# Kernel optimization log

Measured on AMD Instinct MI355X. Metric: run time of the kernel, lower is better.

## Reference

```python
import jax, jax.numpy as jnp
import numpy as np

N = 100_000      # nodes
E = 800_000      # edges (avg degree 8)
IN = 64          # in_channels
OUT = 64         # out_channels
HEADS = 4
HD = OUT // HEADS  # per-head out channels (concat=True)


def _unif(key, shape, fan_in):
    b = 1.0 / np.sqrt(fan_in)
    return jax.random.uniform(key, shape, jnp.float32, -b, b)


def setup_inputs() -> dict:
    key = jax.random.key(0)
    ks = jax.random.split(key, 12)
    x = jax.random.normal(ks[0], (N, IN), jnp.float32)
    pos = jax.random.normal(ks[1], (N, 3), jnp.float32)
    edge_index = jax.random.randint(ks[2], (2, E), 0, N, jnp.int32)
    # Per-head PointTransformerConv params (stacked over heads).
    # lin / lin_src / lin_dst are bias-free Linear(in, hd); pos_nn is Linear(3, hd) with bias.
    W_lin = _unif(ks[3], (HEADS, IN, HD), IN)
    W_src = _unif(ks[4], (HEADS, IN, HD), IN)
    W_dst = _unif(ks[5], (HEADS, IN, HD), IN)
    W_pos = _unif(ks[6], (HEADS, 3, HD), 3)
    b_pos = _unif(ks[7], (HEADS, HD), 3)
    # projection MLP: Linear(OUT,OUT) -> ReLU -> Linear(OUT,OUT)
    W1 = _unif(ks[8], (OUT, OUT), OUT)
    b1 = _unif(ks[9], (OUT,), OUT)
    W2 = _unif(ks[10], (OUT, OUT), OUT)
    b2 = _unif(ks[11], (OUT,), OUT)
    return dict(x=x, pos=pos, edge_index=edge_index, W_lin=W_lin, W_src=W_src,
                W_dst=W_dst, W_pos=W_pos, b_pos=b_pos, W1=W1, b1=b1, W2=W2, b2=b2)


def reference(x, pos, edge_index, W_lin, W_src, W_dst, W_pos, b_pos, W1, b1, W2, b2):
    # Add self-loops (PointTransformerConv default add_self_loops=True).
    loops = jnp.arange(N, dtype=edge_index.dtype)
    src = jnp.concatenate([edge_index[0], loops])   # j (source)
    dst = jnp.concatenate([edge_index[1], loops])   # i (target)

    # Per-node, all-heads projections: [N, H, HD]
    v = jnp.einsum('ni,hio->nho', x, W_lin)
    a_src = jnp.einsum('ni,hio->nho', x, W_src)
    a_dst = jnp.einsum('ni,hio->nho', x, W_dst)

    # Relative-position encoding delta = pos_nn(pos_i - pos_j): [Et, H, HD]
    rel = pos[dst] - pos[src]
    delta = jnp.einsum('ec,hco->eho', rel, W_pos) + b_pos

    # Attention logits per edge/channel: alpha_i - alpha_j + delta
    alpha = a_dst[dst] - a_src[src] + delta

    # Segment softmax over incoming edges of each target node (numerically stable).
    amax = jax.ops.segment_max(alpha, dst, num_segments=N)
    amax = jnp.where(jnp.isfinite(amax), amax, 0.0)
    ex = jnp.exp(alpha - amax[dst])
    denom = jax.ops.segment_sum(ex, dst, num_segments=N)
    attn = ex / jnp.maximum(denom[dst], 1e-16)

    # Message = attn * (lin(x_j) + delta), scatter-sum to targets: [N, H, HD]
    msg = attn * (v[src] + delta)
    out_h = jax.ops.segment_sum(msg, dst, num_segments=N)

    # Concat heads -> projection MLP
    out = out_h.reshape(N, HEADS * HD)
    h = jax.nn.relu(out @ W1 + b1)
    return h @ W2 + b2
```

## Files before the change

kernel.cpp:

```cpp
#include <hip/hip_runtime.h>
#include <math.h>


typedef _Float16 f16;
typedef _Float16 f16x2 __attribute__((ext_vector_type(2)));
typedef _Float16 f16x4 __attribute__((ext_vector_type(4)));
typedef _Float16 f16x8 __attribute__((ext_vector_type(8)));
typedef float f32x4 __attribute__((ext_vector_type(4)));

#define A_PITCH 104
#define C_PITCH 136
#define LOG2E 1.44269504f
#define S_CAP 32

__global__ __launch_bounds__(256) void zero_wprep_kernel(
    int Zb, int* __restrict__ cnt, int N,
    const float* __restrict__ Ws, const float* __restrict__ Wl,
    const float* __restrict__ Wp,
    const float* __restrict__ W1, const float* __restrict__ W2,
    f16* __restrict__ Bt, f16* __restrict__ W1p, f16* __restrict__ W2p,
    f16* __restrict__ AV)
{
    if ((int)blockIdx.x < Zb) {
        int i4 = (blockIdx.x * 256 + threadIdx.x) * 4;
        if (i4 + 3 < N) {
            *(int4*)&cnt[i4] = make_int4(0, 0, 0, 0);
        } else {
            for (int i = i4; i < N; i++) cnt[i] = 0;
        }
        return;
    }
    int idx = (blockIdx.x - Zb) * 256 + threadIdx.x;
    if (idx < 128 * 96) {
        int col = idx / 96, k = idx - col * 96;
        float v = 0.f;
        int p = col >> 1, h = p >> 4, o = p & 15;
        if (col & 1) {
            if (k < 64)      v = Wl[h * 1024 + k * 16 + o];
            else if (k < 67) v = -Wp[h * 48 + (k - 64) * 16 + o];
        } else {
            if (k < 64)      v = -LOG2E * Ws[h * 1024 + k * 16 + o];
            else if (k < 67) v = -LOG2E * Wp[h * 48 + (k - 64) * 16 + o];
        }
        Bt[col * 96 + k] = (f16)v;
    } else if (idx < 128 * 96 + 4096) {
        int t = idx - 128 * 96;
        int col = t >> 6, k = t & 63;
        W1p[col * 64 + k] = (f16)W1[k * 64 + col];
    } else if (idx < 128 * 96 + 8192) {
        int t = idx - 128 * 96 - 4096;
        int col = t >> 6, k = t & 63;
        W2p[col * 64 + k] = (f16)W2[k * 64 + col];
    } else if (idx < 128 * 96 + 8192 + 16) {
        int t = idx - 128 * 96 - 8192;
        f16x8 z = {(f16)0, (f16)0, (f16)0, (f16)0, (f16)0, (f16)0, (f16)0, (f16)0};
        *(f16x8*)&AV[(size_t)N * 128 + t * 8] = z;
    }
}

__global__ __launch_bounds__(256) void gemm_hist_kernel(
    const float* __restrict__ x, const float* __restrict__ pos,
    const f16* __restrict__ Bt,
    f16* __restrict__ AV, int N, int Gb,
    const int* __restrict__ ei, int E, int Hb2,
    int* __restrict__ cnt, int* __restrict__ ssrc)
{
    __shared__ f16 smem[64 * C_PITCH];
    int tid = threadIdx.x;

    if (blockIdx.x & 1) {
        int hb = blockIdx.x >> 1;
        if (hb >= Hb2) return;
        int e0 = hb * 512 + tid;
        int e1 = e0 + 256;
        int s0 = 0, d0 = 0, s1 = 0, d1 = 0;
        bool a0 = e0 < E, a1 = e1 < E;
        if (a0) { s0 = ei[e0]; d0 = ei[E + e0]; }
        if (a1) { s1 = ei[e1]; d1 = ei[E + e1]; }
        if (a0) {
            int r = atomicAdd(&cnt[d0], 1);
            if (r < S_CAP) ssrc[d0 * S_CAP + r] = s0;
        }
        if (a1) {
            int r = atomicAdd(&cnt[d1], 1);
            if (r < S_CAP) ssrc[d1 * S_CAP + r] = s1;
        }
        return;
    }

    int gb = blockIdx.x >> 1;
    if (gb >= Gb) return;
    int l = tid & 63, wv = tid >> 6;
    int quad = l >> 4, lr = l & 15;
    int nb = gb * 64;

    for (int it = 0; it < 4; it++) {
        int q = it * 256 + tid;
        int n = q >> 4, k = (q & 15) * 4;
        float4 xv = make_float4(0.f, 0.f, 0.f, 0.f);
        if (nb + n < N) xv = *(const float4*)&x[(size_t)(nb + n) * 64 + k];
        f16x4 h4; h4[0] = (f16)xv.x; h4[1] = (f16)xv.y; h4[2] = (f16)xv.z; h4[3] = (f16)xv.w;
        *(f16x4*)&smem[n * A_PITCH + k] = h4;
    }
    {
        int n = tid >> 2, seg = tid & 3;
        f16x4 z = {(f16)0, (f16)0, (f16)0, (f16)0};
        f16x4 h4 = z;
        if (seg == 0 && nb + n < N) {
            h4[0] = (f16)pos[(size_t)(nb + n) * 3 + 0];
            h4[1] = (f16)pos[(size_t)(nb + n) * 3 + 1];
            h4[2] = (f16)pos[(size_t)(nb + n) * 3 + 2];
            h4[3] = (f16)1.0f;
        }
        *(f16x4*)&smem[n * A_PITCH + 64 + seg * 8] = h4;
        *(f16x4*)&smem[n * A_PITCH + 64 + seg * 8 + 4] = z;
    }
    __syncthreads();

    f16x8 af[4][3];
    #pragma unroll
    for (int mt = 0; mt < 4; mt++)
        #pragma unroll
        for (int kt = 0; kt < 3; kt++)
            af[mt][kt] = *(const f16x8*)&smem[(mt * 16 + lr) * A_PITCH + kt * 32 + quad * 8];
    __syncthreads();

    #pragma unroll
    for (int t = 0; t < 2; t++) {
        int colBase = (wv * 2 + t) * 16;
        f16x8 b0 = *(const f16x8*)&Bt[(colBase + lr) * 96 + 0  + quad * 8];
        f16x8 b1 = *(const f16x8*)&Bt[(colBase + lr) * 96 + 32 + quad * 8];
        f16x8 b2 = *(const f16x8*)&Bt[(colBase + lr) * 96 + 64 + quad * 8];
        #pragma unroll
        for (int mt = 0; mt < 4; mt++) {
            f32x4 acc = {0.f, 0.f, 0.f, 0.f};
            acc = __builtin_amdgcn_mfma_f32_16x16x32_f16(af[mt][0], b0, acc, 0, 0, 0);
            acc = __builtin_amdgcn_mfma_f32_16x16x32_f16(af[mt][1], b1, acc, 0, 0, 0);
            acc = __builtin_amdgcn_mfma_f32_16x16x32_f16(af[mt][2], b2, acc, 0, 0, 0);
            int col = colBase + lr;
            #pragma unroll
            for (int r = 0; r < 4; r++) {
                int row = mt * 16 + quad * 4 + r;
                smem[row * C_PITCH + col] = (f16)acc[r];
            }
        }
    }
    __syncthreads();

    for (int it = 0; it < 4; it++) {
        int cid = it * 256 + tid;
        int row = cid >> 4, off = (cid & 15) * 8;
        if (nb + row < N) {
            f16x8 w8 = *(const f16x8*)&smem[row * C_PITCH + off];
            f16x8 o;
            #pragma unroll
            for (int p = 0; p < 4; p++) {
                float e  = __builtin_amdgcn_exp2f((float)w8[2 * p]);
                float ev = e * (float)w8[2 * p + 1];
                o[2 * p]     = (f16)e;
                o[2 * p + 1] = (f16)ev;
            }
            *(f16x8*)&AV[(size_t)(nb + row) * 128 + off] = o;
        }
    }
}

__global__ __launch_bounds__(256) void attn_mlp_kernel(
    const f16* __restrict__ AV,
    const int* __restrict__ cnt, const int* __restrict__ ssrc,
    const float* __restrict__ pos, const float* __restrict__ Wp,
    const float* __restrict__ bp,
    const f16* __restrict__ W1p, const f16* __restrict__ W2p,
    const float* __restrict__ b1, const float* __restrict__ b2,
    float* __restrict__ out, int N)
{
    __shared__ f16 As[32 * 72];
    __shared__ f16 Hs[32 * 72];
    __shared__ int lst[32 * S_CAP];
    __shared__ int ldeg[32];
    int tid = threadIdx.x, c = tid & 63, wv = tid >> 6;
    int quad = c >> 4, lr = c & 15;
    int nb = blockIdx.x * 32;

    {
        int4 v = *(const int4*)&ssrc[(size_t)nb * S_CAP + tid * 4];
        *(int4*)&lst[tid * 4] = v;
        if (tid < 32) {
            int dg = cnt[nb + tid];
            ldeg[tid] = dg > S_CAP ? S_CAP : dg;
        }
    }
    __syncthreads();
    for (int q = tid; q < 32 * S_CAP; q += 256) {
        int r = q >> 5, s = q & 31;
        if (s >= ldeg[r]) lst[q] = N;
    }
    __syncthreads();

    float wpx = Wp[quad * 48 + 0  + lr];
    float wpy = Wp[quad * 48 + 16 + lr];
    float wpz = Wp[quad * 48 + 32 + lr];
    float bpc = bp[c];

    f16x2 kd; kd[0] = (f16)1.0f; kd[1] = (f16)0.0f;
    f16x2 kn; kn[0] = (f16)0.0f; kn[1] = (f16)1.0f;

    const f16x2* AV2 = (const f16x2*)AV;

    for (int pt = 0; pt < 4; pt++) {
        int r0 = wv * 8 + pt * 2, r1 = r0 + 1;
        int i0 = __builtin_amdgcn_readfirstlane(nb + r0);
        int i1 = i0 + 1;
        if (i1 >= N) i1 = N - 1;
        if (i0 >= N) i0 = N - 1;
        int deg0 = __builtin_amdgcn_readfirstlane(ldeg[r0]);
        int deg1 = __builtin_amdgcn_readfirstlane(ldeg[r1]);
        float p0x = pos[i0 * 3 + 0], p0y = pos[i0 * 3 + 1], p0z = pos[i0 * 3 + 2];
        float p1x = pos[i1 * 3 + 0], p1y = pos[i1 * 3 + 1], p1z = pos[i1 * 3 + 2];
        f16x2 sv0 = AV2[(size_t)i0 * 64 + c];
        f16x2 sv1 = AV2[(size_t)i1 * 64 + c];
        float den0 = (float)sv0[0], num0 = (float)sv0[1];
        float den1 = (float)sv1[0], num1 = (float)sv1[1];

        for (int b = 0; b < S_CAP; b += 8) {
            bool g0 = b < deg0, g1 = b < deg1;
            if (!(g0 | g1)) break;
            f16x2 w0[8], w1[8];
            if (g0) {
                #pragma unroll
                for (int s = 0; s < 8; s++) {
                    int jj = __builtin_amdgcn_readfirstlane(lst[r0 * S_CAP + b + s]);
                    w0[s] = AV2[(size_t)jj * 64 + c];
                }
            }
            if (g1) {
                #pragma unroll
                for (int s = 0; s < 8; s++) {
                    int jj = __builtin_amdgcn_readfirstlane(lst[r1 * S_CAP + b + s]);
                    w1[s] = AV2[(size_t)jj * 64 + c];
                }
            }
            if (g0) {
                #pragma unroll
                for (int s = 0; s < 8; s++) {
                    den0 = __builtin_amdgcn_fdot2(w0[s], kd, den0, false);
                    num0 = __builtin_amdgcn_fdot2(w0[s], kn, num0, false);
                }
            }
            if (g1) {
                #pragma unroll
                for (int s = 0; s < 8; s++) {
                    den1 = __builtin_amdgcn_fdot2(w1[s], kd, den1, false);
                    num1 = __builtin_amdgcn_fdot2(w1[s], kn, num1, false);
                }
            }
        }
        float Gi0 = p0x * wpx + p0y * wpy + p0z * wpz + bpc;
        float Gi1 = p1x * wpx + p1y * wpy + p1z * wpz + bpc;
        As[r0 * 72 + c] = (f16)(num0 / den0 + Gi0);
        As[r1 * 72 + c] = (f16)(num1 / den1 + Gi1);
    }
    __syncthreads();

    f16x8 af[2][2];
    #pragma unroll
    for (int mt = 0; mt < 2; mt++)
        #pragma unroll
        for (int kt = 0; kt < 2; kt++)
            af[mt][kt] = *(const f16x8*)&As[(mt * 16 + lr) * 72 + kt * 32 + quad * 8];

    int col = wv * 16 + lr;
    f16x8 wb0 = *(const f16x8*)&W1p[col * 64 + quad * 8];
    f16x8 wb1 = *(const f16x8*)&W1p[col * 64 + 32 + quad * 8];
    float bias1 = b1[col];
    #pragma unroll
    for (int mt = 0; mt < 2; mt++) {
        f32x4 acc = {0.f, 0.f, 0.f, 0.f};
        acc = __builtin_amdgcn_mfma_f32_16x16x32_f16(af[mt][0], wb0, acc, 0, 0, 0);
        acc = __builtin_amdgcn_mfma_f32_16x16x32_f16(af[mt][1], wb1, acc, 0, 0, 0);
        #pragma unroll
        for (int r = 0; r < 4; r++) {
            int row = mt * 16 + quad * 4 + r;
            Hs[row * 72 + col] = (f16)fmaxf(acc[r] + bias1, 0.f);
        }
    }
    __syncthreads();

    f16x8 ag[2][2];
    #pragma unroll
    for (int mt = 0; mt < 2; mt++)
        #pragma unroll
        for (int kt = 0; kt < 2; kt++)
            ag[mt][kt] = *(const f16x8*)&Hs[(mt * 16 + lr) * 72 + kt * 32 + quad * 8];

    f16x8 wc0 = *(const f16x8*)&W2p[col * 64 + quad * 8];
    f16x8 wc1 = *(const f16x8*)&W2p[col * 64 + 32 + quad * 8];
    float bias2 = b2[col];
    #pragma unroll
    for (int mt = 0; mt < 2; mt++) {
        f32x4 acc = {0.f, 0.f, 0.f, 0.f};
        acc = __builtin_amdgcn_mfma_f32_16x16x32_f16(ag[mt][0], wc0, acc, 0, 0, 0);
        acc = __builtin_amdgcn_mfma_f32_16x16x32_f16(ag[mt][1], wc1, acc, 0, 0, 0);
        #pragma unroll
        for (int r = 0; r < 4; r++) {
            int row = nb + mt * 16 + quad * 4 + r;
            if (row < N) out[(size_t)row * 64 + col] = acc[r] + bias2;
        }
    }
}

extern "C" void kernel_launch(void* const* d_in, const int* in_sizes, int n_in,
                              void* d_out, int out_size, void* d_ws, size_t ws_size,
                              hipStream_t stream)
{
    const float* x    = (const float*)d_in[0];
    const float* pos  = (const float*)d_in[1];
    const int*   ei   = (const int*)d_in[2];
    const float* Wl   = (const float*)d_in[3];
    const float* Ws   = (const float*)d_in[4];
    const float* Wp   = (const float*)d_in[6];
    const float* bpos = (const float*)d_in[7];
    const float* W1   = (const float*)d_in[8];
    const float* b1   = (const float*)d_in[9];
    const float* W2   = (const float*)d_in[10];
    const float* b2   = (const float*)d_in[11];
    float* out = (float*)d_out;

    const int N = in_sizes[0] / 64;
    const int E = in_sizes[2] / 2;

    char* w = (char*)d_ws;
    f16*  AV   = (f16*)w;                   w += (size_t)(N + 1) * 128 * 2;
    f16*  Bt   = (f16*)w;                   w += 128 * 96 * 2;
    f16*  W1p  = (f16*)w;                   w += 4096 * 2;
    f16*  W2p  = (f16*)w;                   w += 4096 * 2;
    int*  cnt  = (int*)w;                   w += (size_t)N * 4;
    int*  ssrc = (int*)w;                   w += (size_t)N * S_CAP * 4;

    const int Zb  = (N + 1023) / 1024;
    const int Pb  = (128 * 96 + 8192 + 16 + 255) / 256;
    const int Gb  = (N + 63) / 64;
    const int Hb2 = (E + 511) / 512;
    const int Kb  = (Gb > Hb2 ? Gb : Hb2) * 2;

    zero_wprep_kernel<<<Zb + Pb, 256, 0, stream>>>(Zb, cnt, N, Ws, Wl, Wp,
                                                   W1, W2, Bt, W1p, W2p, AV);
    gemm_hist_kernel<<<Kb, 256, 0, stream>>>(x, pos, Bt, AV, N, Gb,
                                             ei, E, Hb2, cnt, ssrc);
    attn_mlp_kernel<<<(N + 31) / 32, 256, 0, stream>>>(AV, cnt, ssrc, pos, Wp, bpos,
                                                       W1p, W2p, b1, b2, out, N);
}
```

Measured before the change: 175.6 us.

## Partition edge histogram by destination class per XCC with dynamic tile tickets

The edge bucketing blocks now read their XCC id and process destination classes ((d>>5)&3), native class first. They claim 512-edge tiles dynamically through per-class atomic tickets, so each XCC mostly performs atomics and scatters into one quarter of the cnt/ssrc arrays, which is meant to improve L2 locality of the atomics across chiplets. In exchange every block re-reads the destination index array for all four classes (4x dst reads), adds a global ticket atomic and two barriers per tile, and depends on the hardware XCC register mapping.

```diff
diff --git a/kernel.cpp b/kernel.cpp
--- a/kernel.cpp
+++ b/kernel.cpp
@@ -14,7 +14,7 @@
 #define S_CAP 32
 
 __global__ __launch_bounds__(256) void zero_wprep_kernel(
-    int Zb, int* __restrict__ cnt, int N,
+    int Zb, int* __restrict__ cnt, int N, int* __restrict__ tick,
     const float* __restrict__ Ws, const float* __restrict__ Wl,
     const float* __restrict__ Wp,
     const float* __restrict__ W1, const float* __restrict__ W2,
@@ -22,6 +22,7 @@
     f16* __restrict__ AV)
 {
     if ((int)blockIdx.x < Zb) {
+        if (blockIdx.x == 0 && threadIdx.x < 4) tick[threadIdx.x] = 0;
         int i4 = (blockIdx.x * 256 + threadIdx.x) * 4;
         if (i4 + 3 < N) {
             *(int4*)&cnt[i4] = make_int4(0, 0, 0, 0);
@@ -63,7 +64,7 @@
     const f16* __restrict__ Bt,
     f16* __restrict__ AV, int N, int Gb,
     const int* __restrict__ ei, int E, int Hb2,
-    int* __restrict__ cnt, int* __restrict__ ssrc)
+    int* __restrict__ cnt, int* __restrict__ ssrc, int* __restrict__ tick)
 {
     __shared__ f16 smem[64 * C_PITCH];
     int tid = threadIdx.x;
@@ -71,19 +72,37 @@
     if (blockIdx.x & 1) {
         int hb = blockIdx.x >> 1;
         if (hb >= Hb2) return;
-        int e0 = hb * 512 + tid;
-        int e1 = e0 + 256;
-        int s0 = 0, d0 = 0, s1 = 0, d1 = 0;
-        bool a0 = e0 < E, a1 = e1 < E;
-        if (a0) { s0 = ei[e0]; d0 = ei[E + e0]; }
-        if (a1) { s1 = ei[e1]; d1 = ei[E + e1]; }
-        if (a0) {
-            int r = atomicAdd(&cnt[d0], 1);
-            if (r < S_CAP) ssrc[d0 * S_CAP + r] = s0;
-        }
-        if (a1) {
-            int r = atomicAdd(&cnt[d1], 1);
-            if (r < S_CAP) ssrc[d1 * S_CAP + r] = s1;
+        int xcc;
+        asm volatile("s_getreg_b32 %0, hwreg(HW_REG_XCC_ID)" : "=s"(xcc));
+        int native = (xcc >> 1) & 3;
+        volatile int* bc = (volatile int*)smem;
+        for (int p = 0; p < 4; p++) {
+            int cls = (native + p) & 3;
+            for (;;) {
+                if (tid == 0) *bc = atomicAdd(&tick[cls], 1);
+                __syncthreads();
+                int t = *bc;
+                __syncthreads();
+                if (t >= Hb2) break;
+                int e0 = t * 512 + tid;
+                int e1 = e0 + 256;
+                int d0 = -1, d1 = -1;
+                if (e0 < E) d0 = ei[E + e0];
+                if (e1 < E) d1 = ei[E + e1];
+                bool k0 = (d0 >= 0) && (((d0 >> 5) & 3) == cls);
+                bool k1 = (d1 >= 0) && (((d1 >> 5) & 3) == cls);
+                int s0 = 0, s1 = 0;
+                if (k0) s0 = ei[e0];
+                if (k1) s1 = ei[e1];
+                if (k0) {
+                    int r = atomicAdd(&cnt[d0], 1);
+                    if (r < S_CAP) ssrc[d0 * S_CAP + r] = s0;
+                }
+                if (k1) {
+                    int r = atomicAdd(&cnt[d1], 1);
+                    if (r < S_CAP) ssrc[d1 * S_CAP + r] = s1;
+                }
+            }
         }
         return;
     }
@@ -336,6 +355,7 @@
     f16*  W2p  = (f16*)w;                   w += 4096 * 2;
     int*  cnt  = (int*)w;                   w += (size_t)N * 4;
     int*  ssrc = (int*)w;                   w += (size_t)N * S_CAP * 4;
+    int*  tick = (int*)w;                   w += 4 * 4;
 
     const int Zb  = (N + 1023) / 1024;
     const int Pb  = (128 * 96 + 8192 + 16 + 255) / 256;
@@ -343,10 +363,10 @@
     const int Hb2 = (E + 511) / 512;
     const int Kb  = (Gb > Hb2 ? Gb : Hb2) * 2;
 
-    zero_wprep_kernel<<<Zb + Pb, 256, 0, stream>>>(Zb, cnt, N, Ws, Wl, Wp,
+    zero_wprep_kernel<<<Zb + Pb, 256, 0, stream>>>(Zb, cnt, N, tick, Ws, Wl, Wp,
                                                    W1, W2, Bt, W1p, W2p, AV);
     gemm_hist_kernel<<<Kb, 256, 0, stream>>>(x, pos, Bt, AV, N, Gb,
-                                             ei, E, Hb2, cnt, ssrc);
+                                             ei, E, Hb2, cnt, ssrc, tick);
     attn_mlp_kernel<<<(N + 31) / 32, 256, 0, stream>>>(AV, cnt, ssrc, pos, Wp, bpos,
                                                        W1p, W2p, b1, b2, out, N);
 }
```

After: 288.7 us. +64.4%, slower.
